# Optimization experiments

Hardware: AMD Instinct MI355X
Metric: run time of the kernel (lower is better)

The kernel has to match this reference:

```python
import jax, jax.numpy as jnp
import numpy as np

HEADS = 16
SEG = 512


def setup_inputs() -> dict:
    key = jax.random.key(0)
    kx, k1, k2, k3, k4, k5 = jax.random.split(key, 6)
    B, L, D = 4, 8192, 1024
    scale = 1.0 / np.sqrt(D).astype(np.float32)
    return {
        "x": jax.random.normal(kx, (B, L, D), jnp.float32),
        "mask": jnp.ones((B, 1, 1, L), jnp.int32),
        "wq": jax.random.normal(k1, (D, D), jnp.float32) * scale,
        "wk": jax.random.normal(k2, (D, D), jnp.float32) * scale,
        "wv": jax.random.normal(k3, (D, D), jnp.float32) * scale,
        "wo_w": jax.random.normal(k4, (D, D), jnp.float32) * scale,
        "wo_b": jnp.zeros((D,), jnp.float32),
        "betas": jax.random.normal(k5, (1, HEADS, 1, D // HEADS), jnp.float32),
    }


def reference(x, mask, wq, wk, wv, wo_w, wo_b, betas):
    B, L, D = x.shape
    H = HEADS
    dk = D // H
    S = SEG
    nseg = L // S
    inv_sqrt_dk = jnp.asarray(1.0 / np.sqrt(dk), x.dtype)

    def proj(w):  # torch Linear: x @ W^T -> (B,H,L,dk)
        return (x @ w.T).reshape(B, L, H, dk).transpose(0, 2, 1, 3)

    q, k, v = proj(wq), proj(wk), proj(wv)

    # chunk into segments: (nseg, B, H, S, dk)
    def seg(t):
        return t.reshape(B, H, nseg, S, dk).transpose(2, 0, 1, 3, 4)

    qs, ksg, vs = seg(q), seg(k), seg(v)
    ms = mask.reshape(B, 1, 1, nseg, S).transpose(3, 0, 1, 2, 4)  # (nseg,B,1,1,S)

    gate = jax.nn.sigmoid(betas)  # (1,H,1,dk)

    def body(carry, inp):
        mem, z = carry  # mem: (B,H,dk,dk), z: (B,H,dk)
        qg, kg, vg, mg = inp
        # segment-local SDPA
        scores = jnp.einsum("bhsd,bhtd->bhst", qg, kg) * inv_sqrt_dk
        scores = jnp.where(mg == 0, jnp.asarray(-1e9, scores.dtype), scores)
        A_dot = jnp.einsum("bhst,bhtd->bhsd", jax.nn.softmax(scores, axis=-1), vg)
        # memory read with old state
        aq = jax.nn.elu(qg) + 1.0
        denom = jnp.einsum("bhsd,bhd->bhs", aq, z)[..., None] + 1e-9
        A_mem = jnp.einsum("bhsd,bhde->bhse", aq, mem) / denom
        # linear memory update
        ak = jax.nn.elu(kg) + 1.0
        mem = mem + jnp.einsum("bhsd,bhse->bhde", ak, vg)
        z = z + ak.sum(axis=2)
        att = gate * A_mem + (1.0 - gate) * A_dot
        return (mem, z), att

    mem0 = jnp.zeros((B, H, dk, dk), x.dtype)
    z0 = jnp.zeros((B, H, dk), x.dtype)
    _, ys = jax.lax.scan(body, (mem0, z0), (qs, ksg, vs, ms))
    # (nseg,B,H,S,dk) -> (B, L, D)
    out = ys.transpose(1, 0, 3, 2, 4).reshape(B, L, D)
    return out @ wo_w.T + wo_b
```

## Files before the change

kernel.cpp:

```cpp
#include <hip/hip_runtime.h>

typedef float fv2 __attribute__((ext_vector_type(2)));
typedef float fv4 __attribute__((ext_vector_type(4)));
typedef _Float16 hfv8 __attribute__((ext_vector_type(8)));
typedef unsigned short u16v4 __attribute__((ext_vector_type(4)));
typedef unsigned short u16v8 __attribute__((ext_vector_type(8)));
typedef unsigned int u32v4 __attribute__((ext_vector_type(4)));

#define B_DIM 4
#define L_DIM 8192
#define D_DIM 1024
#define H_NUM 16
#define NSEG 16
#define SEG_S 512
#define M_TOK (B_DIM * L_DIM)

__device__ __forceinline__ unsigned short f2h(float f) {
  return __builtin_bit_cast(unsigned short, (_Float16)f);
}
__device__ __forceinline__ float h2f(unsigned short u) {
  return (float)__builtin_bit_cast(_Float16, u);
}
__device__ __forceinline__ unsigned packh2(float v) {
  const _Float16 h = (_Float16)v;
  const unsigned short lb = __builtin_bit_cast(unsigned short, (_Float16)(v - (float)h));
  return (unsigned)__builtin_bit_cast(unsigned short, h) | ((unsigned)lb << 16);
}

__device__ __forceinline__ void unpack8(u32v4 a, u32v4 b, u16v8& hi8, u16v8& lo8) {
  u32v4 hi, lo;
  hi[0] = __builtin_amdgcn_perm(a[1], a[0], 0x05040100u);
  hi[1] = __builtin_amdgcn_perm(a[3], a[2], 0x05040100u);
  hi[2] = __builtin_amdgcn_perm(b[1], b[0], 0x05040100u);
  hi[3] = __builtin_amdgcn_perm(b[3], b[2], 0x05040100u);
  lo[0] = __builtin_amdgcn_perm(a[1], a[0], 0x07060302u);
  lo[1] = __builtin_amdgcn_perm(a[3], a[2], 0x07060302u);
  lo[2] = __builtin_amdgcn_perm(b[1], b[0], 0x07060302u);
  lo[3] = __builtin_amdgcn_perm(b[3], b[2], 0x07060302u);
  hi8 = __builtin_bit_cast(u16v8, hi);
  lo8 = __builtin_bit_cast(u16v8, lo);
}
__device__ __forceinline__ u16v8 hi8of(u32v4 a, u32v4 b) {
  u32v4 hi;
  hi[0] = __builtin_amdgcn_perm(a[1], a[0], 0x05040100u);
  hi[1] = __builtin_amdgcn_perm(a[3], a[2], 0x05040100u);
  hi[2] = __builtin_amdgcn_perm(b[1], b[0], 0x05040100u);
  hi[3] = __builtin_amdgcn_perm(b[3], b[2], 0x05040100u);
  return __builtin_bit_cast(u16v8, hi);
}

__global__ __launch_bounds__(256) void conv_w16(
    const float* __restrict__ in, unsigned short* __restrict__ outp, int n4) {
  int i = blockIdx.x * 256 + threadIdx.x;
  const int stride = gridDim.x * 256;
  for (; i < n4; i += stride) {
    fv4 v = reinterpret_cast<const fv4*>(in)[i];
    u16v4 p;
#pragma unroll
    for (int j = 0; j < 4; ++j) p[j] = f2h(v[j]);
    reinterpret_cast<u16v4*>(outp)[i] = p;
  }
}

template <int OMODE>
__global__ __launch_bounds__(256, 4) void gemm_bt(
    const _Float16* __restrict__ A16, const _Float16* __restrict__ B16,
    float* __restrict__ C, const float* __restrict__ bias,
    unsigned* __restrict__ Cp, unsigned short* __restrict__ Cs,
    int M, int N, int K) {
  __shared__ _Float16 sA[2][4096];
  __shared__ _Float16 sB[2][4096];
  const int tid = threadIdx.x;
  const int lane = tid & 63;
  const int wv = tid >> 6;
  const int wr = wv >> 1, wc = wv & 1;
  const int g = lane >> 4, ln16 = lane & 15;

  const int hw = blockIdx.x;
  const int xcd = hw & 7;
  const int rem = hw >> 3;
  const int ntile = rem & 7;
  const int yhi = rem >> 3;
  const int mtile = yhi * 8 + xcd;
  const int mBase = mtile * 128;
  const int nBase = ntile * 128;

  fv4 acc[4][4] = {};

  const int srow = lane >> 2;
  const int cgx = ((lane & 3) ^ ((lane >> 3) & 3)) * 8;
  const long aStageBase = (long)(mBase + wv * 32 + srow) * K + cgx;
  const long bStageBase = (long)(nBase + wv * 32 + srow) * K + cgx;
  const int rgx = (g ^ ((ln16 >> 1) & 3)) * 8;
  const int arow0 = wr * 64 + ln16;
  const int brow0 = wc * 64 + ln16;

  auto STAGE = [&](int t, int bi) {
#pragma unroll
    for (int i = 0; i < 2; ++i) {
      __builtin_amdgcn_global_load_lds(
          (const __attribute__((address_space(1))) void*)(A16 + aStageBase + (long)i * 16 * K + t * 32),
          (__attribute__((address_space(3))) void*)&sA[bi][wv * 1024 + i * 512], 16, 0, 0);
      __builtin_amdgcn_global_load_lds(
          (const __attribute__((address_space(1))) void*)(B16 + bStageBase + (long)i * 16 * K + t * 32),
          (__attribute__((address_space(3))) void*)&sB[bi][wv * 1024 + i * 512], 16, 0, 0);
    }
  };
  auto COMPUTE = [&](int bi) {
    hfv8 fa[4], fb[4];
#pragma unroll
    for (int i = 0; i < 4; ++i) {
      fa[i] = *(const hfv8*)&sA[bi][(arow0 + i * 16) * 32 + rgx];
      fb[i] = *(const hfv8*)&sB[bi][(brow0 + i * 16) * 32 + rgx];
    }
#pragma unroll
    for (int i = 0; i < 4; ++i)
#pragma unroll
      for (int j = 0; j < 4; ++j)
        acc[i][j] = __builtin_amdgcn_mfma_f32_16x16x32_f16(fa[i], fb[j], acc[i][j], 0, 0, 0);
  };

  const int NT = K / 32;
  STAGE(0, 0);
  asm volatile("s_waitcnt vmcnt(0)" ::: "memory");
  __builtin_amdgcn_s_barrier();
  for (int t = 0; t < NT; t += 2) {
    STAGE(t + 1, 1);
    COMPUTE(0);
    asm volatile("s_waitcnt vmcnt(0) lgkmcnt(0)" ::: "memory");
    __builtin_amdgcn_s_barrier();
    if (t + 2 < NT) STAGE(t + 2, 0);
    COMPUTE(1);
    asm volatile("s_waitcnt vmcnt(0) lgkmcnt(0)" ::: "memory");
    __builtin_amdgcn_s_barrier();
  }

  const int crow0 = mBase + wr * 64 + ((lane >> 4) << 2);
  const int ccol0 = nBase + wc * 64 + (lane & 15);
#pragma unroll
  for (int j = 0; j < 4; ++j) {
    const int col = ccol0 + j * 16;
    float bv = 0.f;
    if (OMODE == 0) bv = bias ? bias[col] : 0.f;
#pragma unroll
    for (int i = 0; i < 4; ++i) {
      const long rb = (long)(crow0 + i * 16) * N + col;
#pragma unroll
      for (int r = 0; r < 4; ++r) {
        if (OMODE == 0) C[rb + (long)r * N] = acc[i][j][r] + bv;
        else if (OMODE == 1) Cp[rb + (long)r * N] = packh2(acc[i][j][r]);
        else Cs[rb + (long)r * N] = f2h(acc[i][j][r]);
      }
    }
  }
}

__global__ __launch_bounds__(256) void seg_outer_mfma(
    const unsigned* __restrict__ Kp, const unsigned short* __restrict__ V16,
    float* __restrict__ U, float* __restrict__ Zs) {
  __shared__ _Float16 sAh[64 * 64], sAl[64 * 64];
  __shared__ _Float16 sVh[64 * 64];
  __shared__ float sZf[64];
  const int bid = blockIdx.x;
  const int b = bid >> 8, seg = (bid >> 4) & 15, h = bid & 15;
  const int tid = threadIdx.x;
  const int lane = tid & 63, w = tid >> 6;
  const int g = lane >> 4, ln16 = lane & 15;
  const long base = ((long)b * L_DIM + (long)seg * SEG_S) * D_DIM + h * 64;

  if (tid < 64) sZf[tid] = 0.f;
  fv4 acc[4] = {};
  float zacc = 0.f;
  const int strow = tid & 63;
  const int sg0 = (tid >> 6) * 16;
  const int wsw = (strow & 7) << 3;
  const int rsw = (ln16 & 7) << 3;

  for (int c = 0; c < 8; ++c) {
    __syncthreads();
#pragma unroll
    for (int jj = 0; jj < 2; ++jj) {
      u16v8 ah, al, vh;
#pragma unroll
      for (int i = 0; i < 8; ++i) {
        const long gidx = base + (long)(c * 64 + sg0 + jj * 8 + i) * D_DIM + strow;
        const unsigned ku = Kp[gidx];
        const float kv = h2f((unsigned short)(ku & 0xffffu)) +
                         h2f((unsigned short)(ku >> 16));
        const float a = kv > 0.f ? kv + 1.f : __expf(kv);
        zacc += a;
        const unsigned short hb = f2h(a);
        ah[i] = hb;
        al[i] = f2h(a - h2f(hb));
        vh[i] = V16[gidx];
      }
      const int col = (sg0 + jj * 8) ^ wsw;
      *(u16v8*)&sAh[strow * 64 + col] = ah;
      *(u16v8*)&sAl[strow * 64 + col] = al;
      *(u16v8*)&sVh[strow * 64 + col] = vh;
    }
    __syncthreads();
#pragma unroll
    for (int kf = 0; kf < 2; ++kf) {
      const int so = (kf * 32 + g * 8) ^ rsw;
      hfv8 aH = *(const hfv8*)&sAh[(w * 16 + ln16) * 64 + so];
      hfv8 aL = *(const hfv8*)&sAl[(w * 16 + ln16) * 64 + so];
#pragma unroll
      for (int et = 0; et < 4; ++et) {
        hfv8 bH = *(const hfv8*)&sVh[(et * 16 + ln16) * 64 + so];
        acc[et] = __builtin_amdgcn_mfma_f32_16x16x32_f16(aH, bH, acc[et], 0, 0, 0);
        acc[et] = __builtin_amdgcn_mfma_f32_16x16x32_f16(aL, bH, acc[et], 0, 0, 0);
      }
    }
  }
  atomicAdd(&sZf[strow], zacc);
  __syncthreads();

  const long ub = (long)bid * 4096;
#pragma unroll
  for (int et = 0; et < 4; ++et)
#pragma unroll
    for (int r = 0; r < 4; ++r)
      U[ub + (long)(w * 16 + g * 4 + r) * 64 + et * 16 + ln16] = acc[et][r];
  if (tid < 64) Zs[(long)bid * 64 + tid] = sZf[tid];
}

__global__ __launch_bounds__(256) void seg_prefix(
    const float* __restrict__ U, const float* __restrict__ Zs,
    float* __restrict__ Mem, float* __restrict__ Zp) {
  const int bh = blockIdx.x;
  const int b = bh >> 4, h = bh & 15;
  const int jc = blockIdx.y;
  const int tid = threadIdx.x;
  for (int j = jc * 512 + tid; j < jc * 512 + 512; j += 256) {
    float run = 0.f;
#pragma unroll
    for (int t = 0; t < NSEG; ++t) {
      const long idx = ((long)(b * 256 + t * 16 + h)) * 4096 + j;
      Mem[idx] = run;
      run += U[idx];
    }
  }
  if (jc == 0 && tid < 64) {
    float run = 0.f;
#pragma unroll
    for (int t = 0; t < NSEG; ++t) {
      const long idx = ((long)(b * 256 + t * 16 + h)) * 64 + tid;
      Zp[idx] = run;
      run += Zs[idx];
    }
  }
}

__global__ __launch_bounds__(512, 4) void attn_seg_mfma(
    const unsigned* __restrict__ Qp, const unsigned* __restrict__ Kp,
    const unsigned short* __restrict__ V16, const int* __restrict__ mask,
    const float* __restrict__ Mem, const float* __restrict__ Zp,
    const float* __restrict__ betas, unsigned short* __restrict__ Op16, int b) {
  __shared__ _Float16 sKh[64 * 72];
  __shared__ _Float16 sVTh[64 * 64];
  __shared__ _Float16 sP[8][16 * 72];
  __shared__ float sMadd[64], sZ[64], sGate[64];

  const int bx = (blockIdx.x & 7) * 128 + (blockIdx.x >> 3);
  const int qblk = bx & 3, h = (bx >> 2) & 15, seg = bx >> 6;
  const int shb = b * 256 + seg * 16 + h;
  const int tid = threadIdx.x;
  const int lane = tid & 63, w = tid >> 6;
  const int g = lane >> 4, ln16 = lane & 15;
  const int rsw = (ln16 & 7) << 3;

  const int qglob = b * L_DIM + seg * SEG_S + qblk * 128 + w * 16 + ln16;
  const long qbase = (long)qglob * D_DIM + h * 64;
  hfv8 qh[2], ql[2];
#pragma unroll
  for (int dt = 0; dt < 2; ++dt) {
    u32v4 a = *(const u32v4*)&Qp[qbase + dt * 32 + g * 8];
    u32v4 bb = *(const u32v4*)&Qp[qbase + dt * 32 + g * 8 + 4];
    u16v8 hi8, lo8;
    unpack8(a, bb, hi8, lo8);
    qh[dt] = __builtin_bit_cast(hfv8, hi8);
    ql[dt] = __builtin_bit_cast(hfv8, lo8);
  }

  fv4 O[4] = {};
  float m_run = -1e30f, l_run = 0.f;
  const long kvbase0 = ((long)b * L_DIM + (long)seg * SEG_S) * D_DIM + h * 64;

  for (int c = 0; c < 8; ++c) {
    __syncthreads();
    {
      const int row = tid >> 3, d0 = (tid & 7) * 8;
      const long ga = kvbase0 + (long)(c * 64 + row) * D_DIM + d0;
      u32v4 a = *(const u32v4*)&Kp[ga], bb = *(const u32v4*)&Kp[ga + 4];
      *(u16v8*)&sKh[row * 72 + d0] = hi8of(a, bb);
    }
    {
      const int e = tid & 63, kg = (tid >> 6) * 8;
      u16v8 hv;
#pragma unroll
      for (int j = 0; j < 8; ++j)
        hv[j] = V16[kvbase0 + (long)(c * 64 + kg + j) * D_DIM + e];
      *(u16v8*)&sVTh[e * 64 + (kg ^ ((e & 7) << 3))] = hv;
    }
    if (tid < 64)
      sMadd[tid] = (mask[b * L_DIM + seg * SEG_S + c * 64 + tid] == 0) ? -1e9f : 0.f;
    __syncthreads();

    fv4 madd[4];
#pragma unroll
    for (int kt = 0; kt < 4; ++kt) madd[kt] = *(const fv4*)&sMadd[kt * 16 + g * 4];

    fv4 sc[4];
#pragma unroll
    for (int kt = 0; kt < 4; ++kt) {
      const int ro = (kt * 16 + ln16) * 72 + g * 8;
      hfv8 kh0 = *(const hfv8*)&sKh[ro], kh1 = *(const hfv8*)&sKh[ro + 32];
      fv4 s = {};
      s = __builtin_amdgcn_mfma_f32_16x16x32_f16(kh0, qh[0], s, 0, 0, 0);
      s = __builtin_amdgcn_mfma_f32_16x16x32_f16(kh1, qh[1], s, 0, 0, 0);
      s = __builtin_amdgcn_mfma_f32_16x16x32_f16(kh0, ql[0], s, 0, 0, 0);
      s = __builtin_amdgcn_mfma_f32_16x16x32_f16(kh1, ql[1], s, 0, 0, 0);
      sc[kt] = s;
    }
    float pmax = -3.0e38f;
#pragma unroll
    for (int kt = 0; kt < 4; ++kt)
#pragma unroll
      for (int r = 0; r < 4; ++r) {
        const float v = __builtin_fmaf(sc[kt][r], 0.125f, madd[kt][r]);
        sc[kt][r] = v;
        pmax = fmaxf(pmax, v);
      }
    pmax = fmaxf(pmax, __shfl_xor(pmax, 16));
    pmax = fmaxf(pmax, __shfl_xor(pmax, 32));
    if (pmax > m_run + 8.f) {
      const float resc = __expf(m_run - pmax);
      l_run *= resc;
#pragma unroll
      for (int et = 0; et < 4; ++et)
#pragma unroll
        for (int r = 0; r < 4; ++r) O[et][r] *= resc;
      m_run = pmax;
    }
    float psum = 0.f;
#pragma unroll
    for (int kt = 0; kt < 4; ++kt) {
      u16v4 pv;
#pragma unroll
      for (int r = 0; r < 4; ++r) {
        const unsigned short hb = f2h(__expf(sc[kt][r] - m_run));
        pv[r] = hb;
        psum += h2f(hb);
      }
      *(u16v4*)&sP[w][ln16 * 72 + kt * 16 + g * 4] = pv;
    }
    psum += __shfl_xor(psum, 16);
    psum += __shfl_xor(psum, 32);
    l_run += psum;

    hfv8 pf0 = *(const hfv8*)&sP[w][ln16 * 72 + g * 8];
    hfv8 pf1 = *(const hfv8*)&sP[w][ln16 * 72 + 32 + g * 8];
#pragma unroll
    for (int et = 0; et < 4; ++et) {
      const int rb = (et * 16 + ln16) * 64;
      hfv8 vh0 = *(const hfv8*)&sVTh[rb + ((g * 8) ^ rsw)];
      hfv8 vh1 = *(const hfv8*)&sVTh[rb + ((g * 8 + 32) ^ rsw)];
      fv4 o = O[et];
      o = __builtin_amdgcn_mfma_f32_16x16x32_f16(vh0, pf0, o, 0, 0, 0);
      o = __builtin_amdgcn_mfma_f32_16x16x32_f16(vh1, pf1, o, 0, 0, 0);
      O[et] = o;
    }
  }

  __syncthreads();
  {
    const int e2 = (tid & 31) * 2, d4 = (tid >> 5) * 4;
    const float* Memp = Mem + (long)shb * 4096;
    fv2 ld[4];
#pragma unroll
    for (int i = 0; i < 4; ++i) ld[i] = *(const fv2*)&Memp[(d4 + i) * 64 + e2];
#pragma unroll
    for (int je = 0; je < 2; ++je) {
      u16v4 hv;
#pragma unroll
      for (int i = 0; i < 4; ++i) hv[i] = f2h(ld[i][je]);
      *(u16v4*)&sKh[(e2 + je) * 72 + d4] = hv;
    }
  }
  if (tid < 64) {
    sZ[tid] = Zp[(long)shb * 64 + tid];
    sGate[tid] = 1.f / (1.f + __expf(-betas[h * 64 + tid]));
  }
  __syncthreads();

  float dpart = 0.f;
#pragma unroll
  for (int dt = 0; dt < 2; ++dt) {
    u16v8 ah, al;
#pragma unroll
    for (int j = 0; j < 8; ++j) {
      const float x = (float)qh[dt][j] + (float)ql[dt][j];
      const float a = x > 0.f ? x + 1.f : __expf(x);
      dpart += a * sZ[dt * 32 + g * 8 + j];
      const unsigned short hb = f2h(a);
      ah[j] = hb;
      al[j] = f2h(a - h2f(hb));
    }
    qh[dt] = __builtin_bit_cast(hfv8, ah);
    ql[dt] = __builtin_bit_cast(hfv8, al);
  }
  dpart += __shfl_xor(dpart, 16);
  dpart += __shfl_xor(dpart, 32);
  const float invden = 1.f / (dpart + 1e-9f);
  const float invl = 1.f / l_run;

  const long obase = (long)qglob * D_DIM + h * 64;
#pragma unroll
  for (int et = 0; et < 4; ++et) {
    const int ro = (et * 16 + ln16) * 72 + g * 8;
    hfv8 mh0 = *(const hfv8*)&sKh[ro], mh1 = *(const hfv8*)&sKh[ro + 32];
    fv4 o = {};
    o = __builtin_amdgcn_mfma_f32_16x16x32_f16(mh0, qh[0], o, 0, 0, 0);
    o = __builtin_amdgcn_mfma_f32_16x16x32_f16(mh1, qh[1], o, 0, 0, 0);
    o = __builtin_amdgcn_mfma_f32_16x16x32_f16(mh0, ql[0], o, 0, 0, 0);
    o = __builtin_amdgcn_mfma_f32_16x16x32_f16(mh1, ql[1], o, 0, 0, 0);
    const fv4 gt = *(const fv4*)&sGate[et * 16 + g * 4];
    u16v4 st;
#pragma unroll
    for (int r = 0; r < 4; ++r) {
      const float att = gt[r] * o[r] * invden + (1.f - gt[r]) * O[et][r] * invl;
      st[r] = f2h(att);
    }
    *(u16v4*)&Op16[obase + et * 16 + g * 4] = st;
  }
}

extern "C" void kernel_launch(void* const* d_in, const int* in_sizes, int n_in,
                              void* d_out, int out_size, void* d_ws, size_t ws_size,
                              hipStream_t stream) {
  (void)in_sizes; (void)n_in; (void)out_size;
  const float* x     = (const float*)d_in[0];
  const int*   mask  = (const int*)d_in[1];
  const float* wq    = (const float*)d_in[2];
  const float* wk    = (const float*)d_in[3];
  const float* wv    = (const float*)d_in[4];
  const float* wo    = (const float*)d_in[5];
  const float* wob   = (const float*)d_in[6];
  const float* betas = (const float*)d_in[7];
  float* out = (float*)d_out;

  const size_t TOK = (size_t)M_TOK * D_DIM;
  char* ws = (char*)d_ws;
  size_t off = 0;
  auto alloc = [&](size_t bytes) {
    char* p = ws + off;
    off += (bytes + 255) & ~(size_t)255;
    return p;
  };
  unsigned short* w16[4];
  for (int i = 0; i < 4; ++i)
    w16[i] = (unsigned short*)alloc((size_t)D_DIM * D_DIM * 2);
  unsigned short* x16 = (unsigned short*)alloc(TOK * 2);
  unsigned* qp = (unsigned*)alloc(TOK * 4);
  unsigned* kp = (unsigned*)alloc(TOK * 4);
  unsigned short* vp16 = (unsigned short*)alloc(TOK * 2);
  float* U   = (float*)alloc((size_t)B_DIM * NSEG * H_NUM * 4096 * 4);
  float* Mem = (float*)alloc((size_t)B_DIM * NSEG * H_NUM * 4096 * 4);
  float* Zs  = (float*)alloc((size_t)B_DIM * NSEG * H_NUM * 64 * 4);
  float* Zp  = (float*)alloc((size_t)B_DIM * NSEG * H_NUM * 64 * 4);
  unsigned short* att16 = x16;

  if (off > ws_size) return;

  const float* wsrc[4] = {wq, wk, wv, wo};
  for (int i = 0; i < 4; ++i)
    conv_w16<<<256, 256, 0, stream>>>(wsrc[i], w16[i], D_DIM * D_DIM / 4);
  conv_w16<<<2048, 256, 0, stream>>>(x, x16, (int)(TOK / 4));

  const int ggrid = (D_DIM / 128) * (M_TOK / 128);
  gemm_bt<1><<<ggrid, 256, 0, stream>>>(
      (const _Float16*)x16, (const _Float16*)w16[0], nullptr, nullptr, qp, nullptr,
      M_TOK, D_DIM, D_DIM);
  gemm_bt<1><<<ggrid, 256, 0, stream>>>(
      (const _Float16*)x16, (const _Float16*)w16[1], nullptr, nullptr, kp, nullptr,
      M_TOK, D_DIM, D_DIM);
  gemm_bt<2><<<ggrid, 256, 0, stream>>>(
      (const _Float16*)x16, (const _Float16*)w16[2], nullptr, nullptr, nullptr, vp16,
      M_TOK, D_DIM, D_DIM);

  seg_outer_mfma<<<B_DIM * NSEG * H_NUM, 256, 0, stream>>>(kp, vp16, U, Zs);
  seg_prefix<<<dim3(B_DIM * H_NUM, 8), 256, 0, stream>>>(U, Zs, Mem, Zp);

  for (int b = 0; b < B_DIM; ++b)
    attn_seg_mfma<<<NSEG * H_NUM * 4, 512, 0, stream>>>(qp, kp, vp16, mask, Mem, Zp,
                                                        betas, att16, b);

  gemm_bt<0><<<ggrid, 256, 0, stream>>>(
      (const _Float16*)att16, (const _Float16*)w16[3], out, wob, nullptr, nullptr,
      M_TOK, D_DIM, D_DIM);
}
```

Baseline: 709.2 us.

## Fuse Q/K/V projections into one GEMM and triple-buffer LDS pipeline

Concatenates the fp16 Q, K and V weights into one 3072-row matrix so a single GEMM launch computes all three projections, routing each output tile to the Q, K or V buffer in the epilogue. The GEMM mainloop moves from a double-buffered loop with two full barriers per pair of steps to a three-stage LDS ring with a partial vmcnt wait, so loads run two steps ahead. This removes two launches and lets the three projections share one wave schedule over the same x tiles. In exchange, the extra LDS buffer lowers the occupancy bound from 4 to 3 blocks per CU.

```diff
diff --git a/kernel.cpp b/kernel.cpp
--- a/kernel.cpp
+++ b/kernel.cpp
@@ -62,14 +62,14 @@
   }
 }
 
-template <int OMODE>
-__global__ __launch_bounds__(256, 4) void gemm_bt(
+template <int QKV>
+__global__ __launch_bounds__(256, 3) void gemm_bt(
     const _Float16* __restrict__ A16, const _Float16* __restrict__ B16,
     float* __restrict__ C, const float* __restrict__ bias,
-    unsigned* __restrict__ Cp, unsigned short* __restrict__ Cs,
-    int M, int N, int K) {
-  __shared__ _Float16 sA[2][4096];
-  __shared__ _Float16 sB[2][4096];
+    unsigned* __restrict__ Qp, unsigned* __restrict__ Kp,
+    unsigned short* __restrict__ Vs, int M, int NTILES, int K) {
+  __shared__ _Float16 sA[3][4096];
+  __shared__ _Float16 sB[3][4096];
   const int tid = threadIdx.x;
   const int lane = tid & 63;
   const int wv = tid >> 6;
@@ -79,11 +79,18 @@
   const int hw = blockIdx.x;
   const int xcd = hw & 7;
   const int rem = hw >> 3;
-  const int ntile = rem & 7;
-  const int yhi = rem >> 3;
+  const int ntile = rem % NTILES;
+  const int yhi = rem / NTILES;
   const int mtile = yhi * 8 + xcd;
   const int mBase = mtile * 128;
   const int nBase = ntile * 128;
+
+  const int ccol0 = nBase + wc * 64 + (lane & 15);
+  float bv[4] = {};
+  if (QKV == 0 && bias) {
+#pragma unroll
+    for (int j = 0; j < 4; ++j) bv[j] = bias[ccol0 + j * 16];
+  }
 
   fv4 acc[4][4] = {};
 
@@ -122,34 +129,46 @@
 
   const int NT = K / 32;
   STAGE(0, 0);
-  asm volatile("s_waitcnt vmcnt(0)" ::: "memory");
-  __builtin_amdgcn_s_barrier();
-  for (int t = 0; t < NT; t += 2) {
-    STAGE(t + 1, 1);
-    COMPUTE(0);
-    asm volatile("s_waitcnt vmcnt(0) lgkmcnt(0)" ::: "memory");
+  STAGE(1, 1);
+  for (int t = 0; t < NT; ++t) {
+    if (t < NT - 1)
+      asm volatile("s_waitcnt vmcnt(4)" ::: "memory");
+    else
+      asm volatile("s_waitcnt vmcnt(0)" ::: "memory");
     __builtin_amdgcn_s_barrier();
-    if (t + 2 < NT) STAGE(t + 2, 0);
-    COMPUTE(1);
-    asm volatile("s_waitcnt vmcnt(0) lgkmcnt(0)" ::: "memory");
-    __builtin_amdgcn_s_barrier();
+    if (t + 2 < NT) STAGE(t + 2, (t + 2) % 3);
+    COMPUTE(t % 3);
+    asm volatile("s_waitcnt lgkmcnt(0)" ::: "memory");
   }
 
   const int crow0 = mBase + wr * 64 + ((lane >> 4) << 2);
-  const int ccol0 = nBase + wc * 64 + (lane & 15);
-#pragma unroll
-  for (int j = 0; j < 4; ++j) {
-    const int col = ccol0 + j * 16;
-    float bv = 0.f;
-    if (OMODE == 0) bv = bias ? bias[col] : 0.f;
-#pragma unroll
-    for (int i = 0; i < 4; ++i) {
-      const long rb = (long)(crow0 + i * 16) * N + col;
-#pragma unroll
-      for (int r = 0; r < 4; ++r) {
-        if (OMODE == 0) C[rb + (long)r * N] = acc[i][j][r] + bv;
-        else if (OMODE == 1) Cp[rb + (long)r * N] = packh2(acc[i][j][r]);
-        else Cs[rb + (long)r * N] = f2h(acc[i][j][r]);
+  if (QKV) {
+    const int which = nBase >> 10;
+    const int colb = ccol0 & 1023;
+    unsigned* dstp = (which == 0) ? Qp : Kp;
+#pragma unroll
+    for (int j = 0; j < 4; ++j) {
+      const int col = colb + j * 16;
+#pragma unroll
+      for (int i = 0; i < 4; ++i) {
+        const long rb = (long)(crow0 + i * 16) * 1024 + col;
+#pragma unroll
+        for (int r = 0; r < 4; ++r) {
+          if (which < 2) dstp[rb + (long)r * 1024] = packh2(acc[i][j][r]);
+          else Vs[rb + (long)r * 1024] = f2h(acc[i][j][r]);
+        }
+      }
+    }
+  } else {
+#pragma unroll
+    for (int j = 0; j < 4; ++j) {
+      const int col = ccol0 + j * 16;
+#pragma unroll
+      for (int i = 0; i < 4; ++i) {
+        const long rb = (long)(crow0 + i * 16) * 1024 + col;
+#pragma unroll
+        for (int r = 0; r < 4; ++r)
+          C[rb + (long)r * 1024] = acc[i][j][r] + bv[j];
       }
     }
   }
@@ -458,9 +477,8 @@
     off += (bytes + 255) & ~(size_t)255;
     return p;
   };
-  unsigned short* w16[4];
-  for (int i = 0; i < 4; ++i)
-    w16[i] = (unsigned short*)alloc((size_t)D_DIM * D_DIM * 2);
+  unsigned short* wqkv16 = (unsigned short*)alloc((size_t)3 * D_DIM * D_DIM * 2);
+  unsigned short* wo16   = (unsigned short*)alloc((size_t)D_DIM * D_DIM * 2);
   unsigned short* x16 = (unsigned short*)alloc(TOK * 2);
   unsigned* qp = (unsigned*)alloc(TOK * 4);
   unsigned* kp = (unsigned*)alloc(TOK * 4);
@@ -473,21 +491,16 @@
 
   if (off > ws_size) return;
 
-  const float* wsrc[4] = {wq, wk, wv, wo};
-  for (int i = 0; i < 4; ++i)
-    conv_w16<<<256, 256, 0, stream>>>(wsrc[i], w16[i], D_DIM * D_DIM / 4);
+  conv_w16<<<256, 256, 0, stream>>>(wq, wqkv16, D_DIM * D_DIM / 4);
+  conv_w16<<<256, 256, 0, stream>>>(wk, wqkv16 + (size_t)D_DIM * D_DIM, D_DIM * D_DIM / 4);
+  conv_w16<<<256, 256, 0, stream>>>(wv, wqkv16 + (size_t)2 * D_DIM * D_DIM, D_DIM * D_DIM / 4);
+  conv_w16<<<256, 256, 0, stream>>>(wo, wo16, D_DIM * D_DIM / 4);
   conv_w16<<<2048, 256, 0, stream>>>(x, x16, (int)(TOK / 4));
 
-  const int ggrid = (D_DIM / 128) * (M_TOK / 128);
-  gemm_bt<1><<<ggrid, 256, 0, stream>>>(
-      (const _Float16*)x16, (const _Float16*)w16[0], nullptr, nullptr, qp, nullptr,
-      M_TOK, D_DIM, D_DIM);
-  gemm_bt<1><<<ggrid, 256, 0, stream>>>(
-      (const _Float16*)x16, (const _Float16*)w16[1], nullptr, nullptr, kp, nullptr,
-      M_TOK, D_DIM, D_DIM);
-  gemm_bt<2><<<ggrid, 256, 0, stream>>>(
-      (const _Float16*)x16, (const _Float16*)w16[2], nullptr, nullptr, nullptr, vp16,
-      M_TOK, D_DIM, D_DIM);
+  const int qkvGrid = 24 * (M_TOK / 128);
+  gemm_bt<1><<<qkvGrid, 256, 0, stream>>>(
+      (const _Float16*)x16, (const _Float16*)wqkv16, nullptr, nullptr,
+      qp, kp, vp16, M_TOK, 24, D_DIM);
 
   seg_outer_mfma<<<B_DIM * NSEG * H_NUM, 256, 0, stream>>>(kp, vp16, U, Zs);
   seg_prefix<<<dim3(B_DIM * H_NUM, 8), 256, 0, stream>>>(U, Zs, Mem, Zp);
@@ -496,7 +509,8 @@
     attn_seg_mfma<<<NSEG * H_NUM * 4, 512, 0, stream>>>(qp, kp, vp16, mask, Mem, Zp,
                                                         betas, att16, b);
 
-  gemm_bt<0><<<ggrid, 256, 0, stream>>>(
-      (const _Float16*)att16, (const _Float16*)w16[3], out, wob, nullptr, nullptr,
-      M_TOK, D_DIM, D_DIM);
-}
+  const int oGrid = 8 * (M_TOK / 128);
+  gemm_bt<0><<<oGrid, 256, 0, stream>>>(
+      (const _Float16*)att16, (const _Float16*)wo16, out, wob,
+      nullptr, nullptr, nullptr, M_TOK, 8, D_DIM);
+}
```

Measured after the change: 751.6 us. +6.0%, slower.
